# Performance work log

Hardware: AMD Instinct MI355X
Metric: run time of the kernel (lower is better)

The kernel has to match this reference:

```python
import jax, jax.numpy as jnp
import numpy as np

R = 3                 # corr_radius
STRIDE = 4
RES = (384, 512)      # model_resolution (H, W)
G = 2 * R + 1         # 7: support grid side


def setup_inputs() -> dict:
    key = jax.random.key(0)
    ks = jax.random.split(key, 16)
    B, S, N, C = 1, 8, 1024, 128
    H0, W0 = RES[0] // STRIDE, RES[1] // STRIDE  # 96, 128
    inp = {}
    for i in range(4):
        h, w = H0 >> i, W0 >> i
        inp[f"fmaps{i}"] = jax.random.normal(ks[i], (B, S, C, h, w), jnp.float32)
        inp[f"track{i}"] = jax.random.normal(ks[4 + i], (B, G * G, N, C), jnp.float32)
    inp["coords"] = jax.random.uniform(ks[8], (B, S, N, 2), jnp.float32) * jnp.asarray([W0 - 1.0, H0 - 1.0], jnp.float32)
    inp["vis"] = jax.random.normal(ks[9], (B, S, N, 1), jnp.float32)
    inp["conf"] = jax.random.normal(ks[10], (B, S, N, 1), jnp.float32)
    r2 = G * G
    inp["w1"] = jax.random.normal(ks[11], (r2 * r2, 384), jnp.float32) * (1.0 / np.sqrt(r2 * r2))
    inp["b1"] = jnp.zeros((384,), jnp.float32)
    inp["w2"] = jax.random.normal(ks[12], (384, 256), jnp.float32) * (1.0 / np.sqrt(384))
    inp["b2"] = jnp.zeros((256,), jnp.float32)
    inp["time_emb"] = jax.random.normal(ks[13], (1, S, 1110), jnp.float32) * 0.02
    return inp


def bilinear_sample(fmap, x, y):
    """fmap: (BT, C, H, W); x, y: (BT, M) pixel coords. Border padding, align_corners=True
    (matches torch grid_sample as used by co-tracker's bilinear_sampler)."""
    BT, C, H, W = fmap.shape
    x0f = jnp.floor(x)
    y0f = jnp.floor(y)
    wx = (x - x0f)[:, None, :]
    wy = (y - y0f)[:, None, :]
    x0 = jnp.clip(x0f.astype(jnp.int32), 0, W - 1)
    x1 = jnp.clip(x0f.astype(jnp.int32) + 1, 0, W - 1)
    y0 = jnp.clip(y0f.astype(jnp.int32), 0, H - 1)
    y1 = jnp.clip(y0f.astype(jnp.int32) + 1, 0, H - 1)
    flat = fmap.reshape(BT, C, H * W)

    def g(yi, xi):
        idx = (yi * W + xi)[:, None, :]  # (BT, 1, M)
        return jnp.take_along_axis(flat, idx, axis=2)  # (BT, C, M)

    return (g(y0, x0) * (1 - wx) * (1 - wy) + g(y0, x1) * wx * (1 - wy)
            + g(y1, x0) * (1 - wx) * wy + g(y1, x1) * wx * wy)


def posenc(x, min_deg=0, max_deg=10):
    scales = jnp.asarray([2.0 ** i for i in range(min_deg, max_deg)], x.dtype)
    xb = (x[..., None, :] * scales[:, None]).reshape(x.shape[:-1] + (-1,))
    four = jnp.sin(jnp.concatenate([xb, xb + 0.5 * jnp.pi], axis=-1))
    return jnp.concatenate([x, four], axis=-1)


def reference(fmaps0, fmaps1, fmaps2, fmaps3, track0, track1, track2, track3,
              coords, vis, conf, w1, b1, w2, b2, time_emb):
    B, S, N, _ = coords.shape
    fps = [fmaps0, fmaps1, fmaps2, fmaps3]
    tps = [track0, track1, track2, track3]
    d = jnp.linspace(-R, R, G)
    xoff, yoff = jnp.meshgrid(d, d, indexing='ij')  # (7,7): rows = x offset, cols = y offset

    embs = []
    for lvl in range(4):
        fm = fps[lvl]
        C, H, W = fm.shape[2], fm.shape[3], fm.shape[4]
        c = coords.reshape(B * S, N, 1, 1, 2) / (2.0 ** lvl)
        x = c[..., 0] + xoff          # (B*S, N, 7, 7)
        y = c[..., 1] + yoff
        M = N * G * G
        sampled = bilinear_sample(fm.reshape(B * S, C, H, W), x.reshape(B * S, M), y.reshape(B * S, M))
        corr_feat = sampled.reshape(B, S, C, N, G, G).transpose(0, 1, 3, 4, 5, 2)  # (B,S,N,7,7,C)
        track = tps[lvl].reshape(B, G, G, N, C).transpose(0, 3, 1, 2, 4)           # (B,N,7,7,C)
        vol = jnp.einsum('btnhwc,bnijc->btnhwij', corr_feat, track)                # (B,S,N,7,7,7,7)
        h = jax.nn.gelu(vol.reshape(B * S * N, G * G * G * G) @ w1 + b1, approximate=False)
        embs.append(h @ w2 + b2)
    corr_embs = jnp.concatenate(embs, axis=-1).reshape(B, S, N, -1)  # (B,S,N,1024)

    rel_f = jnp.pad(coords[:, :-1] - coords[:, 1:], ((0, 0), (0, 1), (0, 0), (0, 0)))
    rel_b = jnp.pad(coords[:, 1:] - coords[:, :-1], ((0, 0), (1, 0), (0, 0), (0, 0)))
    scale = jnp.asarray([RES[1], RES[0]], jnp.float32) / STRIDE
    rel_emb = posenc(jnp.concatenate([rel_f / scale, rel_b / scale], axis=-1))  # (B,S,N,84)

    x = jnp.concatenate([vis, conf, corr_embs, rel_emb], axis=-1)  # (B,S,N,1110)
    x = x.transpose(0, 2, 1, 3).reshape(B * N, S, -1) + time_emb
    return x.reshape(B, N, S, -1)
```

## Files before the change

kernel.cpp:

```cpp
#include <hip/hip_runtime.h>
#include <math.h>


#define SN 8
#define NN 1024
#define CC 128
#define K1P2 2752
#define H1 384
#define H2 256
#define DOUT 1110

typedef short bf16x8 __attribute__((ext_vector_type(8)));
typedef short s16x4 __attribute__((ext_vector_type(4)));
typedef float f32x4 __attribute__((ext_vector_type(4)));

__device__ inline unsigned short f2b(float x) {
    union { float f; unsigned u; } v; v.f = x;
    unsigned r = v.u + 0x7FFFu + ((v.u >> 16) & 1u);
    return (unsigned short)(r >> 16);
}
__device__ inline float b2f(unsigned short u) {
    union { unsigned u; float f; } v; v.u = (unsigned)u << 16; return v.f;
}
__device__ inline void gll16(const void* g, void* l) {
    __builtin_amdgcn_global_load_lds(
        (const __attribute__((address_space(1))) void*)g,
        (__attribute__((address_space(3))) void*)l, 16, 0, 0);
}
__device__ inline int swz(int row, int g) {
    return row * 128 + ((g ^ (row & 7)) << 3);
}

__global__ __launch_bounds__(256) void conv_fmap_kernel(
    const float* __restrict__ in, unsigned short* __restrict__ outp,
    int H, int W)
{
    const int Hp = H + 8, Wp = W + 8;
    const int s = blockIdx.x / Hp, yp = blockIdx.x % Hp;
    const int y = min(max(yp - 4, 0), H - 1);
    const float* src = in + (size_t)s * CC * H * W + (size_t)y * W;
    unsigned short* dst = outp + ((size_t)s * Hp + yp) * Wp * CC;
    for (int idx = threadIdx.x; idx < Wp * CC; idx += 256) {
        int xp = idx >> 7, c = idx & 127;
        int x = min(max(xp - 4, 0), W - 1);
        dst[idx] = f2b(src[(size_t)c * H * W + x]);
    }
}

__global__ __launch_bounds__(256, 3) void sample_vol_kernel(
    const unsigned short* __restrict__ fq0, const unsigned short* __restrict__ fq1,
    const unsigned short* __restrict__ fq2, const unsigned short* __restrict__ fq3,
    const float* __restrict__ tk0, const float* __restrict__ tk1,
    const float* __restrict__ tk2, const float* __restrict__ tk3,
    const float* __restrict__ coords,
    unsigned short* __restrict__ vol,
    int lv0)
{
    __shared__ __align__(16) unsigned short patch[80 * 128];
    __shared__ __align__(16) unsigned short trk[64 * 128];
    __shared__ __align__(16) unsigned short pcL[80 * 68];
    const int n = blockIdx.x & 1023, g = blockIdx.x >> 10;
    const int lvl = lv0 + g;
    const unsigned short* fpad = (lvl == 0) ? fq0 : (lvl == 1) ? fq1
                               : (lvl == 2) ? fq2 : fq3;
    const float* track = (lvl == 0) ? tk0 : (lvl == 1) ? tk1
                       : (lvl == 2) ? tk2 : tk3;
    const int Wp = (128 >> lvl) + 8;
    const int t = threadIdx.x;
    const int lane = t & 63, wv = t >> 6;
    const int rsub = lane & 15, kq = lane >> 4;
    const float inv = 1.0f / (float)(1 << lvl);
    const size_t plane = (size_t)((96 >> lvl) + 8) * Wp * CC;

    int poff[5], ldso[5];
    #pragma unroll
    for (int i = 0; i < 5; ++i) {
        int task64 = wv * 5 + i;
        int point = task64 * 4 + (lane >> 4);
        int v = point / 10, xs = point - v * 10;
        int j = (lane & 15) ^ (point & 7);
        poff[i] = (v * Wp + xs) * CC + j * 8;
        ldso[i] = task64 * 512;
    }

    float cxa[SN], cya[SN];
    #pragma unroll
    for (int s = 0; s < SN; ++s) {
        float2 c2 = *(const float2*)&coords[((size_t)s * NN + n) * 2];
        cxa[s] = c2.x * inv; cya[s] = c2.y * inv;
    }

    int p0b[2], ij0a[2], tau8[2]; bool vld[2];
    #pragma unroll
    for (int rep = 0; rep < 2; ++rep) {
        int tau = t + rep * 256;
        vld[rep] = (tau < 343);
        int tt = vld[rep] ? tau : 0;
        int ab = tt / 7, blk = tt - 7 * ab;
        int a = ab / 7, b = ab - 7 * a;
        p0b[rep] = b * 10 + a;
        ij0a[rep] = blk * 8;
        tau8[rep] = tt * 8;
    }

    int fx = (int)floorf(cxa[0]), fy = (int)floorf(cya[0]);
    int e = (fx - 3) & ~1;
    {
        const unsigned short* base = fpad + ((fy + 1) * Wp + (e + 4)) * CC;
        #pragma unroll
        for (int i = 0; i < 5; ++i) gll16(base + poff[i], &patch[ldso[i]]);
    }
    for (int task = t; task < 49 * 16; task += 256) {
        int row = task >> 4, gg = task & 15;
        const float* srcp = &track[((size_t)row * NN + n) * CC + gg * 8];
        float4 f0 = *(const float4*)srcp;
        float4 f1 = *(const float4*)(srcp + 4);
        bf16x8 v8;
        v8[0] = f2b(f0.x); v8[1] = f2b(f0.y); v8[2] = f2b(f0.z); v8[3] = f2b(f0.w);
        v8[4] = f2b(f1.x); v8[5] = f2b(f1.y); v8[6] = f2b(f1.z); v8[7] = f2b(f1.w);
        *(bf16x8*)&trk[swz(row, gg)] = v8;
    }
    {
        unsigned* T32 = (unsigned*)trk;
        for (int i = t; i < 15 * 64; i += 256) T32[49 * 64 + i] = 0;
    }
    asm volatile("s_waitcnt lgkmcnt(0)" ::: "memory");
    __builtin_amdgcn_s_barrier();
    bf16x8 tf[4];
    #pragma unroll
    for (int kk = 0; kk < 4; ++kk)
        tf[kk] = *(const bf16x8*)&trk[swz(wv * 16 + rsub, kk * 4 + kq)];

    #pragma unroll
    for (int sl = 0; sl < SN; ++sl) {
        const float wx = cxa[sl] - (float)fx, wy = cya[sl] - (float)fy;
        const float w00 = (1.f - wx) * (1.f - wy), w10 = wx * (1.f - wy);
        const float w01 = (1.f - wx) * wy,         w11 = wx * wy;
        const int off = fx - 3 - e;

        if (sl == 0)     asm volatile("s_waitcnt vmcnt(0) lgkmcnt(0)" ::: "memory");
        else if (wv < 2) asm volatile("s_waitcnt vmcnt(2) lgkmcnt(0)" ::: "memory");
        else             asm volatile("s_waitcnt vmcnt(1) lgkmcnt(0)" ::: "memory");
        __builtin_amdgcn_sched_barrier(0);
        __builtin_amdgcn_s_barrier();
        __builtin_amdgcn_sched_barrier(0);

        {
            f32x4 acc[5] = {};
            #pragma unroll
            for (int kk = 0; kk < 4; ++kk) {
                int gg = kk * 4 + kq;
                #pragma unroll
                for (int ti = 0; ti < 5; ++ti) {
                    bf16x8 a = *(const bf16x8*)&patch[swz(ti * 16 + rsub, gg)];
                    acc[ti] = __builtin_amdgcn_mfma_f32_16x16x32_bf16(a, tf[kk], acc[ti], 0, 0, 0);
                }
            }
            const int col = wv * 16 + rsub;
            #pragma unroll
            for (int ti = 0; ti < 5; ++ti)
                #pragma unroll
                for (int r = 0; r < 4; ++r)
                    pcL[(ti * 16 + kq * 4 + r) * 68 + col] = f2b(acc[ti][r]);
        }
        asm volatile("s_waitcnt lgkmcnt(0)" ::: "memory");
        __builtin_amdgcn_s_barrier();
        __builtin_amdgcn_sched_barrier(0);

        if (sl + 1 < SN) {
            fx = (int)floorf(cxa[sl + 1]); fy = (int)floorf(cya[sl + 1]);
            e = (fx - 3) & ~1;
            const unsigned short* base =
                fpad + (size_t)(sl + 1) * plane + ((fy + 1) * Wp + (e + 4)) * CC;
            #pragma unroll
            for (int i = 0; i < 5; ++i) gll16(base + poff[i], &patch[ldso[i]]);
        }
        __builtin_amdgcn_sched_barrier(0);

        {
            unsigned short* vrow = vol + ((size_t)(g * SN + sl) * NN + n) * K1P2;
            #pragma unroll
            for (int rep = 0; rep < 2; ++rep) {
                if (vld[rep]) {
                    int base = (p0b[rep] + off) * 68 + ij0a[rep];
                    s16x4 a0 = *(const s16x4*)&pcL[base],       a1 = *(const s16x4*)&pcL[base + 4];
                    s16x4 b0 = *(const s16x4*)&pcL[base + 68],  b1 = *(const s16x4*)&pcL[base + 72];
                    s16x4 c0 = *(const s16x4*)&pcL[base + 680], c1 = *(const s16x4*)&pcL[base + 684];
                    s16x4 d0 = *(const s16x4*)&pcL[base + 748], d1 = *(const s16x4*)&pcL[base + 752];
                    unsigned w[4];
                    #pragma unroll
                    for (int j = 0; j < 4; ++j) {
                        const int e0 = 2 * j, e1 = 2 * j + 1;
                        float v0 = w00 * b2f((unsigned short)(e0 < 4 ? a0[e0 & 3] : a1[e0 & 3]))
                                 + w10 * b2f((unsigned short)(e0 < 4 ? b0[e0 & 3] : b1[e0 & 3]))
                                 + w01 * b2f((unsigned short)(e0 < 4 ? c0[e0 & 3] : c1[e0 & 3]))
                                 + w11 * b2f((unsigned short)(e0 < 4 ? d0[e0 & 3] : d1[e0 & 3]));
                        float v1 = w00 * b2f((unsigned short)(e1 < 4 ? a0[e1 & 3] : a1[e1 & 3]))
                                 + w10 * b2f((unsigned short)(e1 < 4 ? b0[e1 & 3] : b1[e1 & 3]))
                                 + w01 * b2f((unsigned short)(e1 < 4 ? c0[e1 & 3] : c1[e1 & 3]))
                                 + w11 * b2f((unsigned short)(e1 < 4 ? d0[e1 & 3] : d1[e1 & 3]));
                        w[j] = (unsigned)f2b(v0) | ((unsigned)f2b(v1) << 16);
                    }
                    uint4 st; st.x = w[0]; st.y = w[1]; st.z = w[2]; st.w = w[3];
                    *(uint4*)(vrow + tau8[rep]) = st;
                }
            }
        }
    }
}

__global__ __launch_bounds__(256) void zpad_kernel(
    unsigned short* __restrict__ vol, int rows)
{
    int r = blockIdx.x * 256 + threadIdx.x;
    if (r < rows) {
        uint4 z; z.x = 0; z.y = 0; z.z = 0; z.w = 0;
        *(uint4*)(vol + (size_t)r * K1P2 + 2744) = z;
    }
}

__global__ __launch_bounds__(256) void conv_w1_kernel(
    const float* __restrict__ w1, unsigned short* __restrict__ w1t)
{
    __shared__ float tile[32][33];
    const int kb = blockIdx.x * 32, nb = blockIdx.y * 32;
    const int tx = threadIdx.x & 31, ty = threadIdx.x >> 5;
    #pragma unroll
    for (int i = 0; i < 32; i += 8) {
        int kp = kb + ty + i;
        int k = -1;
        if (kp < 2744) {
            int tau = kp >> 3, r = kp & 7;
            int ab = tau / 7, blk = tau - 7 * ab;
            int ij = blk * 8 + r;
            if (ij < 49) k = ab * 49 + ij;
        }
        tile[ty + i][tx] = (k >= 0) ? w1[(size_t)k * H1 + nb + tx] : 0.f;
    }
    __syncthreads();
    #pragma unroll
    for (int i = 0; i < 32; i += 8)
        w1t[(size_t)(nb + ty + i) * K1P2 + kb + tx] = f2b(tile[tx][ty + i]);
}

__global__ __launch_bounds__(256, 3) void gemm1_kernel(
    const unsigned short* __restrict__ A,
    const unsigned short* __restrict__ Bt,
    const float* __restrict__ bias,
    unsigned short* __restrict__ Hout)
{
    __shared__ __align__(16) unsigned short As[3 * 128 * 32];
    __shared__ __align__(16) unsigned short Bs[3 * 128 * 32];
    const int h = blockIdx.x, q = gridDim.x >> 3;
    const int l = (h & 7) * q + (h >> 3);
    const int m0 = (l / 3) * 128, n0 = (l % 3) * 128;
    const int t = threadIdx.x, lane = t & 63, wv = t >> 6;
    const int wm = wv >> 1, wn = wv & 1;
    const int rsub = lane & 15, kq = lane >> 4;

    const int rA0 = t >> 2, sA0 = (t & 3) ^ ((rA0 >> 1) & 3);
    const int rA1 = (t + 256) >> 2, sA1 = ((t + 256) & 3) ^ ((rA1 >> 1) & 3);
    const unsigned short* gA0 = A  + (size_t)(m0 + rA0) * K1P2 + sA0 * 8;
    const unsigned short* gA1 = A  + (size_t)(m0 + rA1) * K1P2 + sA1 * 8;
    const unsigned short* gB0 = Bt + (size_t)(n0 + rA0) * K1P2 + sA0 * 8;
    const unsigned short* gB1 = Bt + (size_t)(n0 + rA1) * K1P2 + sA1 * 8;
    const int chunk0 = (t & ~63) * 8, chunk1 = (256 + (t & ~63)) * 8;

    f32x4 acc[4][4] = {};

    const int NSTEP = K1P2 / 32;
    #pragma unroll
    for (int p = 0; p < 3; ++p) {
        size_t ko = (size_t)p * 32;
        int lb = p * 4096;
        gll16(gA0 + ko, &As[lb + chunk0]); gll16(gA1 + ko, &As[lb + chunk1]);
        gll16(gB0 + ko, &Bs[lb + chunk0]); gll16(gB1 + ko, &Bs[lb + chunk1]);
    }
    int cur = 0;
    for (int st = 0; st < NSTEP; ++st) {
        const int rem = NSTEP - 1 - st;
        if (rem >= 2)      asm volatile("s_waitcnt vmcnt(8)" ::: "memory");
        else if (rem == 1) asm volatile("s_waitcnt vmcnt(4)" ::: "memory");
        else               asm volatile("s_waitcnt vmcnt(0)" ::: "memory");
        __builtin_amdgcn_s_barrier();
        __builtin_amdgcn_sched_barrier(0);
        const int lb = cur * 4096;
        bf16x8 af[4], bfr[4];
        #pragma unroll
        for (int mi = 0; mi < 4; ++mi) {
            int r = wm * 64 + mi * 16 + rsub;
            int phys = r * 4 + (kq ^ ((r >> 1) & 3));
            af[mi] = *(const bf16x8*)&As[lb + phys * 8];
        }
        #pragma unroll
        for (int ni = 0; ni < 4; ++ni) {
            int r = wn * 64 + ni * 16 + rsub;
            int phys = r * 4 + (kq ^ ((r >> 1) & 3));
            bfr[ni] = *(const bf16x8*)&Bs[lb + phys * 8];
        }
        #pragma unroll
        for (int mi = 0; mi < 4; ++mi)
            #pragma unroll
            for (int ni = 0; ni < 4; ++ni)
                acc[mi][ni] = __builtin_amdgcn_mfma_f32_16x16x32_bf16(
                    af[mi], bfr[ni], acc[mi][ni], 0, 0, 0);
        __builtin_amdgcn_sched_barrier(0);
        __builtin_amdgcn_s_barrier();
        __builtin_amdgcn_sched_barrier(0);
        if (st + 3 < NSTEP) {
            size_t ko = (size_t)(st + 3) * 32;
            gll16(gA0 + ko, &As[lb + chunk0]);
            gll16(gA1 + ko, &As[lb + chunk1]);
            gll16(gB0 + ko, &Bs[lb + chunk0]);
            gll16(gB1 + ko, &Bs[lb + chunk1]);
        }
        cur = (cur == 2) ? 0 : cur + 1;
    }
    #pragma unroll
    for (int mi = 0; mi < 4; ++mi) {
        int row = m0 + wm * 64 + mi * 16 + kq * 4;
        #pragma unroll
        for (int ni = 0; ni < 4; ++ni) {
            int col = n0 + wn * 64 + ni * 16 + rsub;
            float bcol = bias[col];
            #pragma unroll
            for (int r = 0; r < 4; ++r) {
                float x = acc[mi][ni][r] + bcol;
                float gg = 0.5f * x * (1.f + erff(x * 0.70710678118654752f));
                Hout[(size_t)(row + r) * H1 + col] = f2b(gg);
            }
        }
    }
}

__global__ __launch_bounds__(256, 3) void gemm2_kernel(
    const unsigned short* __restrict__ A,
    const unsigned short* __restrict__ Bt,
    const float* __restrict__ bias,
    const float* __restrict__ te,
    float* __restrict__ out,
    int lv0)
{
    __shared__ __align__(16) unsigned short As[3 * 128 * 32];
    __shared__ __align__(16) unsigned short Bs[3 * 128 * 32];
    const int h = blockIdx.x, q = gridDim.x >> 3;
    const int l = (h & 7) * q + (h >> 3);
    const int m0 = (l >> 1) * 128, n0 = (l & 1) * 128;
    const int t = threadIdx.x, lane = t & 63, wv = t >> 6;
    const int wm = wv >> 1, wn = wv & 1;
    const int rsub = lane & 15, kq = lane >> 4;

    const int rA0 = t >> 2, sA0 = (t & 3) ^ ((rA0 >> 1) & 3);
    const int rA1 = (t + 256) >> 2, sA1 = ((t + 256) & 3) ^ ((rA1 >> 1) & 3);
    const unsigned short* gA0 = A  + (size_t)(m0 + rA0) * H1 + sA0 * 8;
    const unsigned short* gA1 = A  + (size_t)(m0 + rA1) * H1 + sA1 * 8;
    const unsigned short* gB0 = Bt + (size_t)(n0 + rA0) * H1 + sA0 * 8;
    const unsigned short* gB1 = Bt + (size_t)(n0 + rA1) * H1 + sA1 * 8;
    const int chunk0 = (t & ~63) * 8, chunk1 = (256 + (t & ~63)) * 8;

    f32x4 acc[4][4] = {};

    const int NSTEP = H1 / 32;
    #pragma unroll
    for (int p = 0; p < 3; ++p) {
        size_t ko = (size_t)p * 32;
        int lb = p * 4096;
        gll16(gA0 + ko, &As[lb + chunk0]); gll16(gA1 + ko, &As[lb + chunk1]);
        gll16(gB0 + ko, &Bs[lb + chunk0]); gll16(gB1 + ko, &Bs[lb + chunk1]);
    }
    int cur = 0;
    for (int st = 0; st < NSTEP; ++st) {
        const int rem = NSTEP - 1 - st;
        if (rem >= 2)      asm volatile("s_waitcnt vmcnt(8)" ::: "memory");
        else if (rem == 1) asm volatile("s_waitcnt vmcnt(4)" ::: "memory");
        else               asm volatile("s_waitcnt vmcnt(0)" ::: "memory");
        __builtin_amdgcn_s_barrier();
        __builtin_amdgcn_sched_barrier(0);
        const int lb = cur * 4096;
        bf16x8 af[4], bfr[4];
        #pragma unroll
        for (int mi = 0; mi < 4; ++mi) {
            int r = wm * 64 + mi * 16 + rsub;
            int phys = r * 4 + (kq ^ ((r >> 1) & 3));
            af[mi] = *(const bf16x8*)&As[lb + phys * 8];
        }
        #pragma unroll
        for (int ni = 0; ni < 4; ++ni) {
            int r = wn * 64 + ni * 16 + rsub;
            int phys = r * 4 + (kq ^ ((r >> 1) & 3));
            bfr[ni] = *(const bf16x8*)&Bs[lb + phys * 8];
        }
        #pragma unroll
        for (int mi = 0; mi < 4; ++mi)
            #pragma unroll
            for (int ni = 0; ni < 4; ++ni)
                acc[mi][ni] = __builtin_amdgcn_mfma_f32_16x16x32_bf16(
                    af[mi], bfr[ni], acc[mi][ni], 0, 0, 0);
        __builtin_amdgcn_sched_barrier(0);
        __builtin_amdgcn_s_barrier();
        __builtin_amdgcn_sched_barrier(0);
        if (st + 3 < NSTEP) {
            size_t ko = (size_t)(st + 3) * 32;
            gll16(gA0 + ko, &As[lb + chunk0]);
            gll16(gA1 + ko, &As[lb + chunk1]);
            gll16(gB0 + ko, &Bs[lb + chunk0]);
            gll16(gB1 + ko, &Bs[lb + chunk1]);
        }
        cur = (cur == 2) ? 0 : cur + 1;
    }
    #pragma unroll
    for (int mi = 0; mi < 4; ++mi) {
        int rowb = m0 + wm * 64 + mi * 16 + kq * 4;
        #pragma unroll
        for (int ni = 0; ni < 4; ++ni) {
            int col = n0 + wn * 64 + ni * 16 + rsub;
            float bcol = bias[col];
            #pragma unroll
            for (int r = 0; r < 4; ++r) {
                int row = rowb + r;
                int g = row >> 13, s = (row >> 10) & 7, n = row & 1023;
                int dcol = 2 + (lv0 + g) * H2 + col;
                out[((size_t)n * SN + s) * DOUT + dcol] =
                    acc[mi][ni][r] + bcol + te[s * DOUT + dcol];
            }
        }
    }
}

__global__ __launch_bounds__(256) void conv_t_kernel(
    const float* __restrict__ in, unsigned short* __restrict__ outp,
    int K, int Nw, int Kp)
{
    __shared__ float tile[32][33];
    const int kb = blockIdx.x * 32, nb = blockIdx.y * 32;
    const int tx = threadIdx.x & 31, ty = threadIdx.x >> 5;
    #pragma unroll
    for (int i = 0; i < 32; i += 8) {
        int k = kb + ty + i, nn = nb + tx;
        tile[ty + i][tx] = (k < K && nn < Nw) ? in[(size_t)k * Nw + nn] : 0.f;
    }
    __syncthreads();
    #pragma unroll
    for (int i = 0; i < 32; i += 8) {
        int nn = nb + ty + i, k = kb + tx;
        if (nn < Nw) outp[(size_t)nn * Kp + k] = f2b(tile[tx][ty + i]);
    }
}

__global__ __launch_bounds__(128) void tail_kernel(
    const float* __restrict__ coords, const float* __restrict__ vis,
    const float* __restrict__ conf, const float* __restrict__ te,
    float* __restrict__ out)
{
    const int b = blockIdx.x;
    const int n = b >> 3, s = b & 7;
    const int d = threadIdx.x;
    if (d >= 86) return;
    const size_t ob = (size_t)b * DOUT;
    if (d == 0) {
        out[ob + 0] = vis[(size_t)s * NN + n] + te[s * DOUT + 0];
    } else if (d == 1) {
        out[ob + 1] = conf[(size_t)s * NN + n] + te[s * DOUT + 1];
    } else {
        int rd = d - 2;
        float cx = coords[((size_t)s * NN + n) * 2 + 0];
        float cy = coords[((size_t)s * NN + n) * 2 + 1];
        float rfx = 0.f, rfy = 0.f, rbx = 0.f, rby = 0.f;
        if (s < SN - 1) {
            rfx = cx - coords[((size_t)(s + 1) * NN + n) * 2 + 0];
            rfy = cy - coords[((size_t)(s + 1) * NN + n) * 2 + 1];
        }
        if (s > 0) {
            rbx = cx - coords[((size_t)(s - 1) * NN + n) * 2 + 0];
            rby = cy - coords[((size_t)(s - 1) * NN + n) * 2 + 1];
        }
        float r4[4] = {rfx / 128.f, rfy / 96.f, rbx / 128.f, rby / 96.f};
        float val;
        if (rd < 4) {
            val = r4[rd];
        } else if (rd < 44) {
            int q = rd - 4; int deg = q >> 2, comp = q & 3;
            val = sinf(r4[comp] * (float)(1 << deg));
        } else {
            int q = rd - 44; int deg = q >> 2, comp = q & 3;
            val = sinf(r4[comp] * (float)(1 << deg) + 1.57079632679489662f);
        }
        int od = 1026 + rd;
        out[ob + od] = val + te[s * DOUT + od];
    }
}

extern "C" void kernel_launch(void* const* d_in, const int* in_sizes, int n_in,
                              void* d_out, int out_size, void* d_ws, size_t ws_size,
                              hipStream_t stream) {
    const float* fmaps[4] = {(const float*)d_in[0], (const float*)d_in[2],
                             (const float*)d_in[4], (const float*)d_in[6]};
    const float* track[4] = {(const float*)d_in[1], (const float*)d_in[3],
                             (const float*)d_in[5], (const float*)d_in[7]};
    const float* coords = (const float*)d_in[8];
    const float* vis    = (const float*)d_in[9];
    const float* conf   = (const float*)d_in[10];
    const float* w1     = (const float*)d_in[11];
    const float* b1     = (const float*)d_in[12];
    const float* w2     = (const float*)d_in[13];
    const float* b2     = (const float*)d_in[14];
    const float* te     = (const float*)d_in[15];
    float* out = (float*)d_out;

    const int Hs[4] = {96, 48, 24, 12};
    const int Ws[4] = {128, 64, 32, 16};

    char* wsb = (char*)d_ws;
    unsigned short* w1t = (unsigned short*)wsb;
    size_t off = (size_t)H1 * K1P2 * 2;
    unsigned short* w2t = (unsigned short*)(wsb + off);
    off += (size_t)H2 * H1 * 2;
    unsigned short* fpad[4];
    for (int l = 0; l < 4; ++l) {
        fpad[l] = (unsigned short*)(wsb + off);
        off += (size_t)SN * (Hs[l] + 8) * (Ws[l] + 8) * CC * 2;
    }
    off += 512;
    const size_t fixed = off;
    int n_lv = 4;
    while (n_lv > 1 &&
           fixed + (size_t)n_lv * SN * NN * (K1P2 + H1) * 2 > ws_size)
        n_lv >>= 1;
    unsigned short* volb = (unsigned short*)(wsb + fixed);
    unsigned short* hb   = volb + (size_t)n_lv * SN * NN * K1P2;

    conv_w1_kernel<<<dim3(K1P2 / 32, H1 / 32), 256, 0, stream>>>(w1, w1t);
    conv_t_kernel<<<dim3(H1 / 32, H2 / 32), 256, 0, stream>>>(w2, w2t, H1, H2, H1);
    for (int l = 0; l < 4; ++l)
        conv_fmap_kernel<<<SN * (Hs[l] + 8), 256, 0, stream>>>(
            fmaps[l], fpad[l], Hs[l], Ws[l]);
    zpad_kernel<<<(n_lv * SN * NN + 255) / 256, 256, 0, stream>>>(
        volb, n_lv * SN * NN);

    for (int lv0 = 0; lv0 < 4; lv0 += n_lv) {
        sample_vol_kernel<<<n_lv * NN, 256, 0, stream>>>(
            fpad[0], fpad[1], fpad[2], fpad[3],
            track[0], track[1], track[2], track[3],
            coords, volb, lv0);
        const int rows = n_lv * SN * NN;
        gemm1_kernel<<<(rows / 128) * 3, 256, 0, stream>>>(volb, w1t, b1, hb);
        gemm2_kernel<<<(rows / 128) * 2, 256, 0, stream>>>(hb, w2t, b2, te, out, lv0);
    }
    tail_kernel<<<SN * NN, 128, 0, stream>>>(coords, vis, conf, te, out);
}
```

Measured before the change: 346.0 us.

## Double-buffer feature patches in sample_vol and raise MFMA wave priority

The sample/volume kernel now keeps two patch buffers and prefetches frame sl+2 while frame sl is computed. The track tile is moved into registers first so its shared-memory buffer can be reused as the second patch buffer. Per-frame floor and offset values are precomputed, and the vmcnt waits are retuned for the deeper pipeline. s_setprio is also raised around MFMA loops in the sample and GEMM kernels so matrix work gets issue priority. The change adds an extra barrier and more in-flight loads, which can raise register pressure.

```diff
diff --git a/kernel.cpp b/kernel.cpp
--- a/kernel.cpp
+++ b/kernel.cpp
@@ -56,8 +56,8 @@
     unsigned short* __restrict__ vol,
     int lv0)
 {
-    __shared__ __align__(16) unsigned short patch[80 * 128];
-    __shared__ __align__(16) unsigned short trk[64 * 128];
+    __shared__ __align__(16) unsigned short bufA[80 * 128];
+    __shared__ __align__(16) unsigned short bufB[80 * 128];
     __shared__ __align__(16) unsigned short pcL[80 * 68];
     const int n = blockIdx.x & 1023, g = blockIdx.x >> 10;
     const int lvl = lv0 + g;
@@ -84,10 +84,14 @@
     }
 
     float cxa[SN], cya[SN];
+    int fxa[SN], fya[SN], ea[SN];
     #pragma unroll
     for (int s = 0; s < SN; ++s) {
         float2 c2 = *(const float2*)&coords[((size_t)s * NN + n) * 2];
         cxa[s] = c2.x * inv; cya[s] = c2.y * inv;
+        fxa[s] = (int)floorf(cxa[s]);
+        fya[s] = (int)floorf(cya[s]);
+        ea[s] = (fxa[s] - 3) & ~1;
     }
 
     int p0b[2], ij0a[2], tau8[2]; bool vld[2];
@@ -103,12 +107,11 @@
         tau8[rep] = tt * 8;
     }
 
-    int fx = (int)floorf(cxa[0]), fy = (int)floorf(cya[0]);
-    int e = (fx - 3) & ~1;
     {
-        const unsigned short* base = fpad + ((fy + 1) * Wp + (e + 4)) * CC;
-        #pragma unroll
-        for (int i = 0; i < 5; ++i) gll16(base + poff[i], &patch[ldso[i]]);
+        const unsigned short* base =
+            fpad + ((fya[0] + 1) * Wp + (ea[0] + 4)) * CC;
+        #pragma unroll
+        for (int i = 0; i < 5; ++i) gll16(base + poff[i], &bufA[ldso[i]]);
     }
     for (int task = t; task < 49 * 16; task += 256) {
         int row = task >> 4, gg = task & 15;
@@ -118,44 +121,67 @@
         bf16x8 v8;
         v8[0] = f2b(f0.x); v8[1] = f2b(f0.y); v8[2] = f2b(f0.z); v8[3] = f2b(f0.w);
         v8[4] = f2b(f1.x); v8[5] = f2b(f1.y); v8[6] = f2b(f1.z); v8[7] = f2b(f1.w);
-        *(bf16x8*)&trk[swz(row, gg)] = v8;
+        *(bf16x8*)&bufB[swz(row, gg)] = v8;
     }
     {
-        unsigned* T32 = (unsigned*)trk;
+        unsigned* T32 = (unsigned*)bufB;
         for (int i = t; i < 15 * 64; i += 256) T32[49 * 64 + i] = 0;
     }
     asm volatile("s_waitcnt lgkmcnt(0)" ::: "memory");
+    __builtin_amdgcn_sched_barrier(0);
     __builtin_amdgcn_s_barrier();
     bf16x8 tf[4];
     #pragma unroll
     for (int kk = 0; kk < 4; ++kk)
-        tf[kk] = *(const bf16x8*)&trk[swz(wv * 16 + rsub, kk * 4 + kq)];
+        tf[kk] = *(const bf16x8*)&bufB[swz(wv * 16 + rsub, kk * 4 + kq)];
+    asm volatile("s_waitcnt lgkmcnt(0)" ::: "memory");
+    __builtin_amdgcn_sched_barrier(0);
+    __builtin_amdgcn_s_barrier();
+    __builtin_amdgcn_sched_barrier(0);
+    {
+        const unsigned short* base =
+            fpad + plane + ((fya[1] + 1) * Wp + (ea[1] + 4)) * CC;
+        #pragma unroll
+        for (int i = 0; i < 5; ++i) gll16(base + poff[i], &bufB[ldso[i]]);
+    }
 
     #pragma unroll
     for (int sl = 0; sl < SN; ++sl) {
-        const float wx = cxa[sl] - (float)fx, wy = cya[sl] - (float)fy;
+        unsigned short* pbuf = (sl & 1) ? bufB : bufA;
+        const float wx = cxa[sl] - (float)fxa[sl], wy = cya[sl] - (float)fya[sl];
         const float w00 = (1.f - wx) * (1.f - wy), w10 = wx * (1.f - wy);
         const float w01 = (1.f - wx) * wy,         w11 = wx * wy;
-        const int off = fx - 3 - e;
-
-        if (sl == 0)     asm volatile("s_waitcnt vmcnt(0) lgkmcnt(0)" ::: "memory");
-        else if (wv < 2) asm volatile("s_waitcnt vmcnt(2) lgkmcnt(0)" ::: "memory");
-        else             asm volatile("s_waitcnt vmcnt(1) lgkmcnt(0)" ::: "memory");
+        const int off = fxa[sl] - 3 - ea[sl];
+
+        if (sl == 0) {
+            asm volatile("s_waitcnt vmcnt(5) lgkmcnt(0)" ::: "memory");
+        } else if (sl == 1) {
+            if (wv < 2) asm volatile("s_waitcnt vmcnt(7) lgkmcnt(0)" ::: "memory");
+            else        asm volatile("s_waitcnt vmcnt(6) lgkmcnt(0)" ::: "memory");
+        } else if (sl == SN - 1) {
+            if (wv < 2) asm volatile("s_waitcnt vmcnt(4) lgkmcnt(0)" ::: "memory");
+            else        asm volatile("s_waitcnt vmcnt(2) lgkmcnt(0)" ::: "memory");
+        } else {
+            if (wv < 2) asm volatile("s_waitcnt vmcnt(9) lgkmcnt(0)" ::: "memory");
+            else        asm volatile("s_waitcnt vmcnt(7) lgkmcnt(0)" ::: "memory");
+        }
         __builtin_amdgcn_sched_barrier(0);
         __builtin_amdgcn_s_barrier();
         __builtin_amdgcn_sched_barrier(0);
 
         {
             f32x4 acc[5] = {};
+            __builtin_amdgcn_s_setprio(1);
             #pragma unroll
             for (int kk = 0; kk < 4; ++kk) {
                 int gg = kk * 4 + kq;
                 #pragma unroll
                 for (int ti = 0; ti < 5; ++ti) {
-                    bf16x8 a = *(const bf16x8*)&patch[swz(ti * 16 + rsub, gg)];
+                    bf16x8 a = *(const bf16x8*)&pbuf[swz(ti * 16 + rsub, gg)];
                     acc[ti] = __builtin_amdgcn_mfma_f32_16x16x32_bf16(a, tf[kk], acc[ti], 0, 0, 0);
                 }
             }
+            __builtin_amdgcn_s_setprio(0);
             const int col = wv * 16 + rsub;
             #pragma unroll
             for (int ti = 0; ti < 5; ++ti)
@@ -167,13 +193,12 @@
         __builtin_amdgcn_s_barrier();
         __builtin_amdgcn_sched_barrier(0);
 
-        if (sl + 1 < SN) {
-            fx = (int)floorf(cxa[sl + 1]); fy = (int)floorf(cya[sl + 1]);
-            e = (fx - 3) & ~1;
+        if (sl + 2 < SN) {
             const unsigned short* base =
-                fpad + (size_t)(sl + 1) * plane + ((fy + 1) * Wp + (e + 4)) * CC;
-            #pragma unroll
-            for (int i = 0; i < 5; ++i) gll16(base + poff[i], &patch[ldso[i]]);
+                fpad + (size_t)(sl + 2) * plane
+                + ((fya[sl + 2] + 1) * Wp + (ea[sl + 2] + 4)) * CC;
+            #pragma unroll
+            for (int i = 0; i < 5; ++i) gll16(base + poff[i], &pbuf[ldso[i]]);
         }
         __builtin_amdgcn_sched_barrier(0);
 
@@ -298,12 +323,14 @@
             int phys = r * 4 + (kq ^ ((r >> 1) & 3));
             bfr[ni] = *(const bf16x8*)&Bs[lb + phys * 8];
         }
+        __builtin_amdgcn_s_setprio(1);
         #pragma unroll
         for (int mi = 0; mi < 4; ++mi)
             #pragma unroll
             for (int ni = 0; ni < 4; ++ni)
                 acc[mi][ni] = __builtin_amdgcn_mfma_f32_16x16x32_bf16(
                     af[mi], bfr[ni], acc[mi][ni], 0, 0, 0);
+        __builtin_amdgcn_s_setprio(0);
         __builtin_amdgcn_sched_barrier(0);
         __builtin_amdgcn_s_barrier();
         __builtin_amdgcn_sched_barrier(0);
@@ -390,12 +417,14 @@
             int phys = r * 4 + (kq ^ ((r >> 1) & 3));
             bfr[ni] = *(const bf16x8*)&Bs[lb + phys * 8];
         }
+        __builtin_amdgcn_s_setprio(1);
         #pragma unroll
         for (int mi = 0; mi < 4; ++mi)
             #pragma unroll
             for (int ni = 0; ni < 4; ++ni)
                 acc[mi][ni] = __builtin_amdgcn_mfma_f32_16x16x32_bf16(
                     af[mi], bfr[ni], acc[mi][ni], 0, 0, 0);
+        __builtin_amdgcn_s_setprio(0);
         __builtin_amdgcn_sched_barrier(0);
         __builtin_amdgcn_s_barrier();
         __builtin_amdgcn_sched_barrier(0);
```

Measured after the change: 342.3 us. Within noise of the previous version (-1.1%).
